# Performance work log

Measured on AMD Instinct MI355X. Metric: run time of the kernel, lower is better.

Reference implementation:

```python
import jax, jax.numpy as jnp
import numpy as np

D_MODEL = 768
D_STATE = 16
D_CONV = 4
EXPAND = 2
D_IN = D_MODEL // 2          # per-direction model dim = 384
D_INNER = EXPAND * D_IN      # ssm inner dim = 768
DT_RANK = (D_IN + 15) // 16  # 24 (mamba 'auto')
B, L = 2, 2048
EPS = 1e-5


def silu(x):
    return x * jax.nn.sigmoid(x)


def layernorm(x, w, b):
    m = jnp.mean(x, axis=-1, keepdims=True)
    v = jnp.var(x, axis=-1, keepdims=True)
    return (x - m) * jax.lax.rsqrt(v + EPS) * w + b


def causal_conv1d(u, w, b):
    # u: (B,L,di), w: (di,K) depthwise causal conv, b: (di,)
    K = w.shape[1]
    up = jnp.pad(u, ((0, 0), (K - 1, 0), (0, 0)))
    Lq = u.shape[1]
    y = sum(up[:, k:k + Lq, :] * w[:, k] for k in range(K))
    return y + b


def mamba_ssm(u, in_w, in_b, conv_w, conv_b, xp_w, dt_w, dt_b, A_log, Dp, out_w, out_b):
    # u: (B,L,D_IN)
    Bz = u.shape[0]
    xz = u @ in_w + in_b                         # (B,L,2*D_INNER)
    x, z = jnp.split(xz, 2, axis=-1)             # (B,L,D_INNER) each
    x = silu(causal_conv1d(x, conv_w, conv_b))
    xd = x @ xp_w                                # (B,L,DT_RANK+2N)
    dt = jax.nn.softplus(xd[..., :DT_RANK] @ dt_w + dt_b)   # (B,L,D_INNER)
    Bm = xd[..., DT_RANK:DT_RANK + D_STATE]      # (B,L,N)
    Cm = xd[..., DT_RANK + D_STATE:]             # (B,L,N)
    A = -jnp.exp(A_log)                          # (D_INNER,N)

    def step(h, xs):
        dt_t, x_t, B_t, C_t = xs                 # (B,di),(B,di),(B,N),(B,N)
        h = jnp.exp(dt_t[..., None] * A) * h + (dt_t * x_t)[..., None] * B_t[:, None, :]
        y = jnp.einsum('bdn,bn->bd', h, C_t)
        return h, y

    h0 = jnp.zeros((Bz, D_INNER, D_STATE), x.dtype)
    xs = (dt.transpose(1, 0, 2), x.transpose(1, 0, 2),
          Bm.transpose(1, 0, 2), Cm.transpose(1, 0, 2))
    _, ys = jax.lax.scan(step, h0, xs)           # ys: (L,B,D_INNER)
    y = ys.transpose(1, 0, 2) + x * Dp
    y = y * silu(z)
    return y @ out_w + out_b                     # (B,L,D_IN)


def setup_inputs() -> dict:
    key = jax.random.key(0)

    def nrm(i, shape, s=0.02):
        return jax.random.normal(jax.random.fold_in(key, i), shape, jnp.float32) * s

    d = {"x": jax.random.normal(jax.random.fold_in(key, 0), (B, L, D_MODEL), jnp.float32)}
    d["in_norm_w"] = jnp.ones(D_MODEL); d["in_norm_b"] = jnp.zeros(D_MODEL)
    d["ip_w"] = nrm(1, (D_MODEL, 2 * D_IN)); d["ip_b"] = jnp.zeros(2 * D_IN)
    i = 10
    for p in ("f", "b"):
        d[p + "_in_w"] = nrm(i, (D_IN, 2 * D_INNER)); d[p + "_in_b"] = jnp.zeros(2 * D_INNER)
        d[p + "_conv_w"] = nrm(i + 1, (D_INNER, D_CONV), 0.2); d[p + "_conv_b"] = jnp.zeros(D_INNER)
        d[p + "_xp_w"] = nrm(i + 2, (D_INNER, DT_RANK + 2 * D_STATE))
        d[p + "_dt_w"] = nrm(i + 3, (DT_RANK, D_INNER), 0.1)
        d[p + "_dt_b"] = nrm(i + 4, (D_INNER,), 0.5)
        d[p + "_A_log"] = jnp.log(jnp.tile(jnp.arange(1, D_STATE + 1, dtype=jnp.float32), (D_INNER, 1)))
        d[p + "_D"] = jnp.ones(D_INNER)
        d[p + "_out_w"] = nrm(i + 5, (D_INNER, D_IN)); d[p + "_out_b"] = jnp.zeros(D_IN)
        i += 10
    d["op_w"] = nrm(30, (2 * D_IN, D_MODEL)); d["op_b"] = jnp.zeros(D_MODEL)
    d["norm_w"] = jnp.ones(D_MODEL); d["norm_b"] = jnp.zeros(D_MODEL)
    return d


def reference(x, in_norm_w, in_norm_b, ip_w, ip_b,
              f_in_w, f_in_b, f_conv_w, f_conv_b, f_xp_w, f_dt_w, f_dt_b, f_A_log, f_D, f_out_w, f_out_b,
              b_in_w, b_in_b, b_conv_w, b_conv_b, b_xp_w, b_dt_w, b_dt_b, b_A_log, b_D, b_out_w, b_out_b,
              op_w, op_b, norm_w, norm_b):
    residual = x
    xn = layernorm(x, in_norm_w, in_norm_b)
    xp = xn @ ip_w + ip_b                        # (B,L,2*D_IN)
    x_fwd, x_bwd = jnp.split(xp, 2, axis=-1)
    out_fwd = mamba_ssm(x_fwd, f_in_w, f_in_b, f_conv_w, f_conv_b, f_xp_w,
                        f_dt_w, f_dt_b, f_A_log, f_D, f_out_w, f_out_b)
    out_bwd = mamba_ssm(jnp.flip(x_bwd, axis=1), b_in_w, b_in_b, b_conv_w, b_conv_b, b_xp_w,
                        b_dt_w, b_dt_b, b_A_log, b_D, b_out_w, b_out_b)
    out_bwd = jnp.flip(out_bwd, axis=1)
    out = jnp.concatenate([out_fwd, out_bwd], axis=-1) @ op_w + op_b
    # dropout is identity in eval mode
    return layernorm(residual + out, norm_w, norm_b)
```

## Files before the change

### kernel.cpp

```cpp
#include <hip/hip_runtime.h>
#include <hip/hip_bf16.h>
#include <math.h>
#include <type_traits>

#define BATCH 2
#define SEQ   2048
#define DMODEL 768
#define DIN   384
#define DINNER 768
#define DSTATE 16
#define DTRANK 24
#define ROWS  (BATCH*SEQ)
#define NCH   64
#define CLEN  (SEQ/NCH)

using short8  = __attribute__((ext_vector_type(8))) short;
using floatx4 = __attribute__((ext_vector_type(4))) float;

__device__ __forceinline__ ushort f2bf(float f) {
    union { float f; uint u; } v; v.f = f;
    uint r = (v.u + 0x7fffu + ((v.u >> 16) & 1u)) >> 16;
    return (ushort)r;
}
__device__ __forceinline__ float bf2f(ushort h) {
    union { uint u; float f; } v; v.u = ((uint)h) << 16;
    return v.f;
}
__device__ __forceinline__ void async16(const ushort* g, ushort* l) {
    __builtin_amdgcn_global_load_lds(
        (const __attribute__((address_space(1))) void*)g,
        (__attribute__((address_space(3))) void*)l,
        16, 0, 0);
}

template<int TM, int TN> struct GemmShT { ushort lA[TM * 64]; ushort lB[TN * 64]; };

template<int TM, int TN>
__device__ __forceinline__ void gemm_accum(
    const ushort* __restrict__ A, int lda,
    const ushort* __restrict__ Bt, int ldb,
    int K, int m0, int n0, GemmShT<TM, TN>& sh,
    floatx4 (&acc)[TM / 32][TN / 32])
{
    constexpr int WM = TM / 2, WN = TN / 2;
    constexpr int MT = WM / 16, NT = WN / 16;
    constexpr int AI = TM / 32, BI = TN / 32;
    const int tid = threadIdx.x;
    const int wave = tid >> 6, lane = tid & 63;
    const int wm = wave >> 1, wn = wave & 1;
    const int quad = lane >> 4, l16 = lane & 15;
    const int lrow = lane >> 3, lcol = (lane & 7) * 8;

    for (int k0 = 0; k0 < K; k0 += 64) {
#pragma unroll
        for (int i = 0; i < AI; i++) {
            int rb = (wave * AI + i) * 8;
            async16(A + (size_t)(m0 + rb + lrow) * lda + k0 + lcol, &sh.lA[rb * 64]);
        }
#pragma unroll
        for (int i = 0; i < BI; i++) {
            int rb = (wave * BI + i) * 8;
            async16(Bt + (size_t)(n0 + rb + lrow) * ldb + k0 + lcol, &sh.lB[rb * 64]);
        }
        __syncthreads();
#pragma unroll
        for (int ks = 0; ks < 2; ks++) {
            short8 af[MT], bf[NT];
#pragma unroll
            for (int i = 0; i < MT; i++)
                af[i] = *(const short8*)&sh.lA[(wm * WM + i * 16 + l16) * 64 + ks * 32 + quad * 8];
#pragma unroll
            for (int j = 0; j < NT; j++)
                bf[j] = *(const short8*)&sh.lB[(wn * WN + j * 16 + l16) * 64 + ks * 32 + quad * 8];
#pragma unroll
            for (int i = 0; i < MT; i++)
#pragma unroll
                for (int j = 0; j < NT; j++)
                    acc[i][j] = __builtin_amdgcn_mfma_f32_16x16x32_bf16(af[i], bf[j], acc[i][j], 0, 0, 0);
        }
        __syncthreads();
    }
}

template<int TM, int TN, bool OUT_BF>
__device__ __forceinline__ void gemm_epilogue(
    const float* __restrict__ bias, void* __restrict__ C, int ldc, int N,
    int m0, int n0, floatx4 (&acc)[TM / 32][TN / 32])
{
    constexpr int WM = TM / 2, WN = TN / 2;
    constexpr int MT = WM / 16, NT = WN / 16;
    const int tid = threadIdx.x;
    const int wave = tid >> 6, lane = tid & 63;
    const int wm = wave >> 1, wn = wave & 1;
    const int quad = lane >> 4, l16 = lane & 15;
#pragma unroll
    for (int i = 0; i < MT; i++) {
#pragma unroll
        for (int j = 0; j < NT; j++) {
            int row = m0 + wm * WM + i * 16 + quad * 4;
            int col = n0 + wn * WN + j * 16 + l16;
            if (col < N) {
                float bv = bias ? bias[col] : 0.f;
#pragma unroll
                for (int r = 0; r < 4; r++) {
                    float v = acc[i][j][r] + bv;
                    if (OUT_BF) ((ushort*)C)[(size_t)(row + r) * ldc + col] = f2bf(v);
                    else        ((float*)C)[(size_t)(row + r) * ldc + col] = v;
                }
            }
        }
    }
}

template<int TM, int TN, bool OUT_BF>
__global__ __launch_bounds__(256) void mfma_gemm_k(
    const ushort* __restrict__ A0, const ushort* __restrict__ A1, int lda,
    const ushort* __restrict__ B0, const ushort* __restrict__ B1, int ldb,
    const float* __restrict__ bias0, const float* __restrict__ bias1,
    void* __restrict__ C0, void* __restrict__ C1, int ldc, int N, int K)
{
    __shared__ GemmShT<TM, TN> sh;
    const ushort* A  = blockIdx.z ? A1 : A0;
    const ushort* Bt = blockIdx.z ? B1 : B0;
    const float* bias = blockIdx.z ? bias1 : bias0;
    void* C = blockIdx.z ? C1 : C0;
    floatx4 acc[TM / 32][TN / 32];
#pragma unroll
    for (int i = 0; i < TM / 32; i++)
#pragma unroll
        for (int j = 0; j < TN / 32; j++)
            acc[i][j] = (floatx4){0.f, 0.f, 0.f, 0.f};
    int m0 = blockIdx.y * TM, n0 = blockIdx.x * TN;
    gemm_accum<TM, TN>(A, lda, Bt, ldb, K, m0, n0, sh, acc);
    gemm_epilogue<TM, TN, OUT_BF>(bias, C, ldc, N, m0, n0, acc);
}

template<int TM, int TN>
__global__ __launch_bounds__(256) void outop_kernel(
    const ushort* __restrict__ A0, const ushort* __restrict__ B0,
    const ushort* __restrict__ A1, const ushort* __restrict__ B1,
    const float* __restrict__ bias, float* __restrict__ C,
    int lda, int ldb, int ldc, int N, int K)
{
    __shared__ GemmShT<TM, TN> sh;
    floatx4 acc[TM / 32][TN / 32];
#pragma unroll
    for (int i = 0; i < TM / 32; i++)
#pragma unroll
        for (int j = 0; j < TN / 32; j++)
            acc[i][j] = (floatx4){0.f, 0.f, 0.f, 0.f};
    int m0 = blockIdx.y * TM, n0 = blockIdx.x * TN;
    gemm_accum<TM, TN>(A0, lda, B0, ldb, K, m0, n0, sh, acc);
    gemm_accum<TM, TN>(A1, lda, B1, ldb, K, m0, n0, sh, acc);
    gemm_epilogue<TM, TN, false>(bias, (void*)C, ldc, N, m0, n0, acc);
}

struct LnSh { float ss[4]; float ssq[4]; float m; float rs; };

template<bool OUT_BF>
__device__ __forceinline__ void ln_row(
    int row, const float* __restrict__ x, const float* __restrict__ res,
    const float* __restrict__ w, const float* __restrict__ b,
    void* __restrict__ out, LnSh& sh)
{
    int tid = threadIdx.x;
    const float* xr = x + (size_t)row * DMODEL;
    const float* rr = res ? res + (size_t)row * DMODEL : nullptr;
    float v[3];
    float s = 0.f, sq = 0.f;
#pragma unroll
    for (int j = 0; j < 3; j++) {
        int i = tid + j * 256;
        float val = xr[i];
        if (rr) val += rr[i];
        v[j] = val; s += val; sq += val * val;
    }
#pragma unroll
    for (int off = 32; off; off >>= 1) {
        s  += __shfl_down(s,  off);
        sq += __shfl_down(sq, off);
    }
    int wid = tid >> 6;
    if ((tid & 63) == 0) { sh.ss[wid] = s; sh.ssq[wid] = sq; }
    __syncthreads();
    if (tid == 0) {
        float S  = sh.ss[0] + sh.ss[1] + sh.ss[2] + sh.ss[3];
        float SQ = sh.ssq[0] + sh.ssq[1] + sh.ssq[2] + sh.ssq[3];
        float m  = S * (1.0f / DMODEL);
        float var = SQ * (1.0f / DMODEL) - m * m;
        sh.m = m;
        sh.rs = rsqrtf(var + 1e-5f);
    }
    __syncthreads();
    float m = sh.m, rs = sh.rs;
#pragma unroll
    for (int j = 0; j < 3; j++) {
        int i = tid + j * 256;
        float r = (v[j] - m) * rs * w[i] + b[i];
        if (OUT_BF) ((ushort*)out)[(size_t)row * DMODEL + i] = f2bf(r);
        else        ((float*)out)[(size_t)row * DMODEL + i] = r;
    }
}

__global__ __launch_bounds__(256) void ln2_kernel(
    const float* __restrict__ x, const float* __restrict__ res,
    const float* __restrict__ w, const float* __restrict__ b,
    float* __restrict__ out)
{
    __shared__ LnSh sh;
    ln_row<false>(blockIdx.x, x, res, w, b, (void*)out, sh);
}

struct TD { const float* src; ushort* dst; int K, N, Np, tile0, tk, mode; };
struct PrepArgs {
    TD d[8];
    int ntc;
    const float *x, *in_nw, *in_nb;
    ushort* xn;
};

__global__ __launch_bounds__(256) void prep_kernel(PrepArgs p)
{
    __shared__ union { float tile[32][33]; LnSh l; } sh;
    int bi = blockIdx.x;
    if (bi < p.ntc) {
        int i = 0;
        while (i < 7 && bi >= p.d[i + 1].tile0) i++;
        TD t = p.d[i];
        int local = bi - t.tile0;
        int tki = local % t.tk, tn = local / t.tk;
        int k0 = tki * 32, n0 = tn * 32;
        if (t.mode == 0) {
            int tx = threadIdx.x & 31, ty = threadIdx.x >> 5;
#pragma unroll
            for (int r = ty; r < 32; r += 8) {
                int n = n0 + tx;
                sh.tile[r][tx] = (n < t.N) ? t.src[(size_t)(k0 + r) * t.N + n] : 0.f;
            }
            __syncthreads();
#pragma unroll
            for (int r = ty; r < 32; r += 8) {
                int n = n0 + r, k = k0 + tx;
                t.dst[(size_t)n * t.K + k] = f2bf(sh.tile[tx][r]);
            }
        } else {
#pragma unroll
            for (int e = threadIdx.x; e < 1024; e += 256) {
                int r = e >> 5, c = e & 31;
                size_t o = (size_t)(k0 + r) * t.N + n0 + c;
                t.dst[o] = f2bf(t.src[o]);
            }
        }
    } else {
        ln_row<true>(bi - p.ntc, p.x, (const float*)nullptr, p.in_nw, p.in_nb,
                     (void*)p.xn, sh.l);
    }
}

struct WfArgs {
    const ushort *fin, *bin, *opT, *ipc, *fow, *bow;
    ushort *WzF, *WzB, *WoF, *WoB;
    const float *ip_b, *f_in_b, *b_in_b, *f_out_b, *b_out_b, *op_b;
    const float *f_in_w32, *b_in_w32, *op_w32;
    float *bzf, *bzb, *bo;
};

__global__ __launch_bounds__(256) void wfuse_kernel(WfArgs p)
{
    __shared__ GemmShT<128, 64> sh;
    int t = blockIdx.x;
    if (t < 432) {
        const ushort *A, *Bt; ushort* C; int lda, ldb, m0, n0;
        if (t < 144)      { A = p.fin;       lda = 384; Bt = p.ipc;       ldb = 768; C = p.WzF; int u = t;       m0 = (u / 12) * 128; n0 = (u % 12) * 64; }
        else if (t < 288) { A = p.bin;       lda = 384; Bt = p.ipc + 384; ldb = 768; C = p.WzB; int u = t - 144; m0 = (u / 12) * 128; n0 = (u % 12) * 64; }
        else if (t < 360) { A = p.opT;       lda = 768; Bt = p.fow;       ldb = 384; C = p.WoF; int u = t - 288; m0 = (u / 12) * 128; n0 = (u % 12) * 64; }
        else              { A = p.opT + 384; lda = 768; Bt = p.bow;       ldb = 384; C = p.WoB; int u = t - 360; m0 = (u / 12) * 128; n0 = (u % 12) * 64; }
        floatx4 acc[4][2];
#pragma unroll
        for (int i = 0; i < 4; i++)
#pragma unroll
            for (int j = 0; j < 2; j++)
                acc[i][j] = (floatx4){0.f, 0.f, 0.f, 0.f};
        gemm_accum<128, 64>(A, lda, Bt, ldb, 384, m0, n0, sh, acc);
        gemm_epilogue<128, 64, true>((const float*)nullptr, (void*)C, 768, 768, m0, n0, acc);
    } else if (t < 438) {
        int n = (t - 432) * 256 + threadIdx.x;
        float acc = p.f_in_b[n];
        for (int j = 0; j < 384; j++)
            acc = fmaf(p.ip_b[j], p.f_in_w32[(size_t)j * 1536 + n], acc);
        p.bzf[n] = acc;
    } else if (t < 444) {
        int n = (t - 438) * 256 + threadIdx.x;
        float acc = p.b_in_b[n];
        for (int j = 0; j < 384; j++)
            acc = fmaf(p.ip_b[384 + j], p.b_in_w32[(size_t)j * 1536 + n], acc);
        p.bzb[n] = acc;
    } else {
        int n = (t - 444) * 256 + threadIdx.x;
        float acc = p.op_b[n];
        for (int j = 0; j < 384; j++)
            acc = fmaf(p.f_out_b[j], p.op_w32[(size_t)j * 768 + n], acc);
        for (int j = 0; j < 384; j++)
            acc = fmaf(p.b_out_b[j], p.op_w32[(size_t)(384 + j) * 768 + n], acc);
        p.bo[n] = acc;
    }
}

__global__ __launch_bounds__(256) void conv_silu_kernel(
    const ushort* __restrict__ xzf, const ushort* __restrict__ xzb,
    const float* __restrict__ cwf, const float* __restrict__ cbf,
    const float* __restrict__ cwb, const float* __restrict__ cbb,
    ushort* __restrict__ outf, ushort* __restrict__ outb)
{
    int rev = blockIdx.y;
    const ushort* xz = rev ? xzb : xzf;
    const float* cw = rev ? cwb : cwf;
    const float* cb = rev ? cbb : cbf;
    ushort* out = rev ? outb : outf;

    int idx = blockIdx.x * 256 + threadIdx.x;
    int dg = idx % (DINNER / 8);
    int row = idx / (DINNER / 8);
    int d0 = dg * 8;
    int t = row & (SEQ - 1), b = row >> 11;
    float acc[8];
#pragma unroll
    for (int c = 0; c < 8; c++) acc[c] = cb[d0 + c];
#pragma unroll
    for (int k = 0; k < 4; k++) {
        int ts = rev ? (t + 3 - k) : (t - 3 + k);
        if (ts >= 0 && ts < SEQ) {
            short8 v = *(const short8*)&xz[((size_t)(b * SEQ + ts)) * 1536 + d0];
#pragma unroll
            for (int c = 0; c < 8; c++)
                acc[c] = fmaf(cw[(d0 + c) * 4 + k], bf2f((ushort)v[c]), acc[c]);
        }
    }
    short8 o;
#pragma unroll
    for (int c = 0; c < 8; c++) {
        float sig = 1.f / (1.f + __expf(-acc[c]));
        o[c] = (short)f2bf(acc[c] * sig);
    }
    *(short8*)&out[(size_t)row * DINNER + d0] = o;
}

#define BM 64
#define BN 64
#define BK 16
__global__ __launch_bounds__(256) void dt_gemm_kernel(
    const float* __restrict__ A0f, const float* __restrict__ A1f, int lda,
    const float* __restrict__ W0, const float* __restrict__ W1, int ldw,
    const float* __restrict__ bias0, const float* __restrict__ bias1,
    float* __restrict__ C0f, float* __restrict__ C1f, int ldc, int K)
{
    const float* A = blockIdx.z ? A1f : A0f;
    const float* W = blockIdx.z ? W1 : W0;
    const float* bias = blockIdx.z ? bias1 : bias0;
    float* C = blockIdx.z ? C1f : C0f;

    __shared__ float As[BK][BM + 4];
    __shared__ float Bs[BK][BN + 4];
    int tid = threadIdx.x;
    int m0 = blockIdx.y * BM;
    int n0 = blockIdx.x * BN;
    int tx = tid & 15, ty = tid >> 4;
    float acc[4][4] = {};

    for (int k0 = 0; k0 < K; k0 += BK) {
        {
            int row = tid >> 2;
            int kq  = (tid & 3) * 4;
            const float* ap = A + (size_t)(m0 + row) * lda + k0 + kq;
            As[kq + 0][row] = (k0 + kq + 0 < K) ? ap[0] : 0.f;
            As[kq + 1][row] = (k0 + kq + 1 < K) ? ap[1] : 0.f;
            As[kq + 2][row] = (k0 + kq + 2 < K) ? ap[2] : 0.f;
            As[kq + 3][row] = (k0 + kq + 3 < K) ? ap[3] : 0.f;
        }
        {
            int krow = tid >> 4;
            int col  = (tid & 15) * 4;
            float4 wv = make_float4(0.f, 0.f, 0.f, 0.f);
            if (k0 + krow < K)
                wv = *(const float4*)(W + (size_t)(k0 + krow) * ldw + n0 + col);
            *(float4*)&Bs[krow][col] = wv;
        }
        __syncthreads();
#pragma unroll
        for (int k = 0; k < BK; k++) {
            float a[4], bv[4];
            *(float4*)a  = *(const float4*)&As[k][ty * 4];
            *(float4*)bv = *(const float4*)&Bs[k][tx * 4];
#pragma unroll
            for (int i = 0; i < 4; i++)
#pragma unroll
                for (int j = 0; j < 4; j++)
                    acc[i][j] = fmaf(a[i], bv[j], acc[i][j]);
        }
        __syncthreads();
    }
#pragma unroll
    for (int i = 0; i < 4; i++) {
        int m = m0 + ty * 4 + i;
#pragma unroll
        for (int j = 0; j < 4; j++) {
            int n = n0 + tx * 4 + j;
            float v = acc[i][j] + bias[n];
            v = (v > 20.f) ? v : log1pf(__expf(v));
            C[(size_t)m * ldc + n] = v;
        }
    }
}

template<bool FULL>
__global__ __launch_bounds__(256) void scan_chunk_kernel(
    const float* __restrict__ dtf, const ushort* __restrict__ xcf,
    const float* __restrict__ xdf, const ushort* __restrict__ xzf,
    const float* __restrict__ Alf, const float* __restrict__ Dff,
    const float* __restrict__ dtb, const ushort* __restrict__ xcb,
    const float* __restrict__ xdb, const ushort* __restrict__ xzb,
    const float* __restrict__ Alb, const float* __restrict__ Dbb,
    float* __restrict__ Hloc, float* __restrict__ Wp,
    const float* __restrict__ Hin,
    ushort* __restrict__ yf, ushort* __restrict__ yb)
{
    const int d     = blockIdx.x * 256 + threadIdx.x;
    const int chunk = blockIdx.y;
    const int bz    = blockIdx.z;
    const int dir   = bz >> 1;
    const int bat   = bz & 1;

    const float*  dt = dir ? dtb : dtf;
    const ushort* xc = dir ? xcb : xcf;
    const float*  xd = dir ? xdb : xdf;
    const ushort* xz = dir ? xzb : xzf;
    const float*  Al = dir ? Alb : Alf;
    const float*  Dp = dir ? Dbb : Dff;
    ushort* yo = dir ? yb : yf;

    float a[16];
    {
        const float4* Ap = (const float4*)(Al + (size_t)d * 16);
#pragma unroll
        for (int q = 0; q < 4; q++) {
            float4 v = Ap[q];
            a[q*4+0] = -__expf(v.x); a[q*4+1] = -__expf(v.y);
            a[q*4+2] = -__expf(v.z); a[q*4+3] = -__expf(v.w);
        }
    }
    const float a0 = a[0];
    bool fast = true;
#pragma unroll
    for (int n = 0; n < 16; n++) {
        float ideal = a0 * (float)(n + 1);
        fast = fast && (fabsf(a[n] - ideal) <= 1e-4f * fabsf(ideal) + 1e-7f);
    }

    float h[16];
    if (FULL) {
        size_t base = ((size_t)(bz * NCH + chunk) * DINNER + d) * 16;
#pragma unroll
        for (int q = 0; q < 4; q++) {
            float4 v = *(const float4*)(Hin + base + q * 4);
            h[q*4+0] = v.x; h[q*4+1] = v.y; h[q*4+2] = v.z; h[q*4+3] = v.w;
        }
    } else {
#pragma unroll
        for (int n = 0; n < 16; n++) h[n] = 0.f;
    }

    const float Dd = FULL ? Dp[d] : 0.f;
    float S = 0.f;

    auto run = [&](auto FASTC) {
        constexpr bool FAST = decltype(FASTC)::value;
#pragma unroll 2
        for (int i = 0; i < CLEN; i++) {
            int tl = chunk * CLEN + i;
            int t  = dir ? (SEQ - 1 - tl) : tl;
            size_t r = (size_t)(bat * SEQ + t);
            float dtv = dt[r * DINNER + d];
            float xv  = bf2f(xc[r * DINNER + d]);
            const float* bp = xd + r * 56 + DTRANK;
            float4 B0 = *(const float4*)(bp + 0);
            float4 B1 = *(const float4*)(bp + 4);
            float4 B2 = *(const float4*)(bp + 8);
            float4 B3 = *(const float4*)(bp + 12);
            float Bv[16] = {B0.x,B0.y,B0.z,B0.w, B1.x,B1.y,B1.z,B1.w,
                            B2.x,B2.y,B2.z,B2.w, B3.x,B3.y,B3.z,B3.w};
            float w[16];
            if (FAST) {
                float e1 = __expf(dtv * a0);
                float e2 = e1*e1, e4 = e2*e2, e8 = e4*e4;
                w[0]=e1;      w[1]=e2;      w[2]=e2*e1;   w[3]=e4;
                w[4]=e4*e1;   w[5]=e4*e2;   w[6]=e4*w[2]; w[7]=e8;
                w[8]=e8*e1;   w[9]=e8*e2;   w[10]=e8*w[2];w[11]=e8*e4;
                w[12]=e8*w[4];w[13]=e8*w[5];w[14]=e8*w[6];w[15]=e8*e8;
            } else {
#pragma unroll
                for (int n = 0; n < 16; n++) w[n] = __expf(dtv * a[n]);
            }
            float bx = dtv * xv;
#pragma unroll
            for (int n = 0; n < 16; n++)
                h[n] = fmaf(w[n], h[n], bx * Bv[n]);
            S += dtv;
            if (FULL) {
                const float* cp = bp + DSTATE;
                float4 C0 = *(const float4*)(cp + 0);
                float4 C1 = *(const float4*)(cp + 4);
                float4 C2 = *(const float4*)(cp + 8);
                float4 C3 = *(const float4*)(cp + 12);
                float Cv[16] = {C0.x,C0.y,C0.z,C0.w, C1.x,C1.y,C1.z,C1.w,
                                C2.x,C2.y,C2.z,C2.w, C3.x,C3.y,C3.z,C3.w};
                float y = 0.f;
#pragma unroll
                for (int n = 0; n < 16; n++) y = fmaf(h[n], Cv[n], y);
                float zv = bf2f(xz[r * 1536 + DINNER + d]);
                float sig = 1.f / (1.f + __expf(-zv));
                yo[r * DINNER + d] = f2bf((y + xv * Dd) * (zv * sig));
            }
        }
    };
    if (fast) run(std::true_type{}); else run(std::false_type{});

    if (!FULL) {
        float W[16];
        if (fast) {
            float E1 = __expf(S * a0);
            float E2 = E1*E1, E4 = E2*E2, E8 = E4*E4;
            W[0]=E1;      W[1]=E2;      W[2]=E2*E1;   W[3]=E4;
            W[4]=E4*E1;   W[5]=E4*E2;   W[6]=E4*W[2]; W[7]=E8;
            W[8]=E8*E1;   W[9]=E8*E2;   W[10]=E8*W[2];W[11]=E8*E4;
            W[12]=E8*W[4];W[13]=E8*W[5];W[14]=E8*W[6];W[15]=E8*E8;
        } else {
#pragma unroll
            for (int n = 0; n < 16; n++) W[n] = __expf(S * a[n]);
        }
        size_t base = ((size_t)(bz * NCH + chunk) * DINNER + d) * 16;
#pragma unroll
        for (int q = 0; q < 4; q++) {
            *(float4*)(Hloc + base + q*4) = make_float4(h[q*4+0], h[q*4+1], h[q*4+2], h[q*4+3]);
            *(float4*)(Wp   + base + q*4) = make_float4(W[q*4+0], W[q*4+1], W[q*4+2], W[q*4+3]);
        }
    }
}

__global__ __launch_bounds__(256) void scan_combine(
    const float* __restrict__ Hloc, const float* __restrict__ Wp,
    float* __restrict__ Hin)
{
    int idx = blockIdx.x * 256 + threadIdx.x;
    int bz = idx / (DINNER * 16);
    int rest = idx % (DINNER * 16);
    float hin = 0.f;
#pragma unroll 4
    for (int k = 0; k < NCH; k++) {
        size_t o = (size_t)(bz * NCH + k) * (DINNER * 16) + rest;
        Hin[o] = hin;
        hin = fmaf(Wp[o], hin, Hloc[o]);
    }
}

extern "C" void kernel_launch(void* const* d_in, const int* in_sizes, int n_in,
                              void* d_out, int out_size, void* d_ws, size_t ws_size,
                              hipStream_t stream)
{
    const float* x        = (const float*)d_in[0];
    const float* in_nw    = (const float*)d_in[1];
    const float* in_nb    = (const float*)d_in[2];
    const float* ip_w     = (const float*)d_in[3];
    const float* ip_b     = (const float*)d_in[4];
    const float* f_in_w   = (const float*)d_in[5];
    const float* f_in_b   = (const float*)d_in[6];
    const float* f_conv_w = (const float*)d_in[7];
    const float* f_conv_b = (const float*)d_in[8];
    const float* f_xp_w   = (const float*)d_in[9];
    const float* f_dt_w   = (const float*)d_in[10];
    const float* f_dt_b   = (const float*)d_in[11];
    const float* f_A_log  = (const float*)d_in[12];
    const float* f_D      = (const float*)d_in[13];
    const float* f_out_w  = (const float*)d_in[14];
    const float* f_out_b  = (const float*)d_in[15];
    const float* b_in_w   = (const float*)d_in[16];
    const float* b_in_b   = (const float*)d_in[17];
    const float* b_conv_w = (const float*)d_in[18];
    const float* b_conv_b = (const float*)d_in[19];
    const float* b_xp_w   = (const float*)d_in[20];
    const float* b_dt_w   = (const float*)d_in[21];
    const float* b_dt_b   = (const float*)d_in[22];
    const float* b_A_log  = (const float*)d_in[23];
    const float* b_D      = (const float*)d_in[24];
    const float* b_out_w  = (const float*)d_in[25];
    const float* b_out_b  = (const float*)d_in[26];
    const float* op_w     = (const float*)d_in[27];
    const float* op_b     = (const float*)d_in[28];
    const float* norm_w   = (const float*)d_in[29];
    const float* norm_b   = (const float*)d_in[30];

    size_t off = 0;
    auto alloc = [&](size_t bytes) {
        void* p = (char*)d_ws + off;
        off += (bytes + 255) & ~(size_t)255;
        return p;
    };
    const size_t R = ROWS;
    ushort* xn_bf   = (ushort*)alloc(R * 768 * 2);
    ushort* xz_f_bf = (ushort*)alloc(R * 1536 * 2);
    ushort* xz_b_bf = (ushort*)alloc(R * 1536 * 2);
    ushort* xc_f_bf = (ushort*)alloc(R * 768 * 2);
    ushort* xc_b_bf = (ushort*)alloc(R * 768 * 2);
    float*  xd_f    = (float*)alloc(R * 56 * 4);
    float*  xd_b    = (float*)alloc(R * 56 * 4);
    float*  dt_f    = (float*)alloc(R * 768 * 4);
    float*  dt_b    = (float*)alloc(R * 768 * 4);
    ushort* y_f_bf  = (ushort*)alloc(R * 768 * 2);
    ushort* y_b_bf  = (ushort*)alloc(R * 768 * 2);
    float*  outraw  = (float*)alloc(R * 768 * 4);
    const size_t SCN = (size_t)4 * NCH * DINNER * 16;
    float* Hloc = (float*)alloc(SCN * 4);
    float* Wpb  = (float*)alloc(SCN * 4);
    float* Hin  = (float*)alloc(SCN * 4);
    ushort* Wt_fin = (ushort*)alloc((size_t)1536 * 384 * 2);
    ushort* Wt_bin = (ushort*)alloc((size_t)1536 * 384 * 2);
    ushort* Wt_op  = (ushort*)alloc((size_t)768 * 768 * 2);
    ushort* Wt_fxp = (ushort*)alloc((size_t)64 * 768 * 2);
    ushort* Wt_bxp = (ushort*)alloc((size_t)64 * 768 * 2);
    ushort* ipc    = (ushort*)alloc((size_t)768 * 768 * 2);
    ushort* fow    = (ushort*)alloc((size_t)768 * 384 * 2);
    ushort* bow    = (ushort*)alloc((size_t)768 * 384 * 2);
    ushort* WzF    = (ushort*)alloc((size_t)1536 * 768 * 2);
    ushort* WzB    = (ushort*)alloc((size_t)1536 * 768 * 2);
    ushort* WoF    = (ushort*)alloc((size_t)768 * 768 * 2);
    ushort* WoB    = (ushort*)alloc((size_t)768 * 768 * 2);
    float*  bzf    = (float*)alloc(1536 * 4);
    float*  bzb    = (float*)alloc(1536 * 4);
    float*  bo     = (float*)alloc(768 * 4);

    PrepArgs pa;
    int tile0 = 0, nd = 0;
    auto add = [&](const float* s, ushort* dst, int K, int N, int Np, int mode) {
        int tiles = mode == 0 ? (K / 32) * (Np / 32) : (K / 32) * (N / 32);
        pa.d[nd] = TD{s, dst, K, N, Np, tile0, K / 32, mode};
        tile0 += tiles;
        nd++;
    };
    add(f_in_w,  Wt_fin, 384, 1536, 1536, 0);
    add(b_in_w,  Wt_bin, 384, 1536, 1536, 0);
    add(op_w,    Wt_op,  768, 768, 768, 0);
    add(f_xp_w,  Wt_fxp, 768, 56, 64, 0);
    add(b_xp_w,  Wt_bxp, 768, 56, 64, 0);
    add(ip_w,    ipc,    768, 768, 768, 1);
    add(f_out_w, fow,    768, 384, 384, 1);
    add(b_out_w, bow,    768, 384, 384, 1);
    pa.ntc = tile0;
    pa.x = x; pa.in_nw = in_nw; pa.in_nb = in_nb; pa.xn = xn_bf;
    hipLaunchKernelGGL(prep_kernel, dim3(tile0 + ROWS), dim3(256), 0, stream, pa);

    WfArgs wa;
    wa.fin = Wt_fin; wa.bin = Wt_bin; wa.opT = Wt_op;
    wa.ipc = ipc; wa.fow = fow; wa.bow = bow;
    wa.WzF = WzF; wa.WzB = WzB; wa.WoF = WoF; wa.WoB = WoB;
    wa.ip_b = ip_b; wa.f_in_b = f_in_b; wa.b_in_b = b_in_b;
    wa.f_out_b = f_out_b; wa.b_out_b = b_out_b; wa.op_b = op_b;
    wa.f_in_w32 = f_in_w; wa.b_in_w32 = b_in_w; wa.op_w32 = op_w;
    wa.bzf = bzf; wa.bzb = bzb; wa.bo = bo;
    hipLaunchKernelGGL(wfuse_kernel, dim3(447), dim3(256), 0, stream, wa);

    hipLaunchKernelGGL((mfma_gemm_k<128, 128, true>), dim3(12, 32, 2), dim3(256), 0, stream,
                       xn_bf, xn_bf, 768, WzF, WzB, 768, bzf, bzb,
                       (void*)xz_f_bf, (void*)xz_b_bf, 1536, 1536, 768);

    hipLaunchKernelGGL(conv_silu_kernel, dim3(ROWS * DINNER / 8 / 256, 2), dim3(256), 0, stream,
                       xz_f_bf, xz_b_bf, f_conv_w, f_conv_b, b_conv_w, b_conv_b,
                       xc_f_bf, xc_b_bf);

    hipLaunchKernelGGL((mfma_gemm_k<128, 64, false>), dim3(1, 32, 2), dim3(256), 0, stream,
                       xc_f_bf, xc_b_bf, 768, Wt_fxp, Wt_bxp, 768,
                       (const float*)nullptr, (const float*)nullptr,
                       (void*)xd_f, (void*)xd_b, 56, 56, 768);

    hipLaunchKernelGGL(dt_gemm_kernel, dim3(768 / BN, ROWS / BM, 2), dim3(256), 0, stream,
                       xd_f, xd_b, 56, f_dt_w, b_dt_w, 768, f_dt_b, b_dt_b,
                       dt_f, dt_b, 768, DTRANK);

    hipLaunchKernelGGL((scan_chunk_kernel<false>), dim3(DINNER / 256, NCH, 4), dim3(256), 0, stream,
                       dt_f, xc_f_bf, xd_f, xz_f_bf, f_A_log, f_D,
                       dt_b, xc_b_bf, xd_b, xz_b_bf, b_A_log, b_D,
                       Hloc, Wpb, (const float*)nullptr, (ushort*)nullptr, (ushort*)nullptr);
    hipLaunchKernelGGL(scan_combine, dim3(4 * DINNER * 16 / 256), dim3(256), 0, stream,
                       Hloc, Wpb, Hin);
    hipLaunchKernelGGL((scan_chunk_kernel<true>), dim3(DINNER / 256, NCH, 4), dim3(256), 0, stream,
                       dt_f, xc_f_bf, xd_f, xz_f_bf, f_A_log, f_D,
                       dt_b, xc_b_bf, xd_b, xz_b_bf, b_A_log, b_D,
                       (float*)nullptr, (float*)nullptr, Hin, y_f_bf, y_b_bf);

    hipLaunchKernelGGL((outop_kernel<128, 64>), dim3(12, 32), dim3(256), 0, stream,
                       y_f_bf, WoF, y_b_bf, WoB, bo, outraw, 768, 768, 768, 768, 768);

    hipLaunchKernelGGL(ln2_kernel, dim3(ROWS), dim3(256), 0, stream,
                       x, outraw, norm_w, norm_b, (float*)d_out);
}
```

Baseline: 401.7 us.

## Fold dt projection into x_proj GEMM, swizzle LDS, and rescalarize conv

Precomputes a combined weight (xp_w columns plus xp_w·dt_w) so a single MFMA GEMM produces both xd and the dt pre-activation, with softplus applied in its epilogue. This removes the separate fp32 SIMT dt GEMM launch and its re-read of xd. The GEMM tile loader and LDS reads gain an XOR swizzle meant to avoid shared-memory bank conflicts. The conv+SiLU kernel changes from eight channels per thread with vector loads to one channel per thread, which lowers per-thread work but adds more and narrower memory accesses. Computing dt through bf16 combined weights changes numerical precision.

```diff
diff --git a/kernel.cpp b/kernel.cpp
--- a/kernel.cpp
+++ b/kernel.cpp
@@ -49,7 +49,8 @@
     const int wave = tid >> 6, lane = tid & 63;
     const int wm = wave >> 1, wn = wave & 1;
     const int quad = lane >> 4, l16 = lane & 15;
-    const int lrow = lane >> 3, lcol = (lane & 7) * 8;
+    const int lrow = lane >> 3;
+    const int lcol = ((lane & 7) ^ (lane >> 3)) * 8;
 
     for (int k0 = 0; k0 < K; k0 += 64) {
 #pragma unroll
@@ -67,11 +68,15 @@
         for (int ks = 0; ks < 2; ks++) {
             short8 af[MT], bf[NT];
 #pragma unroll
-            for (int i = 0; i < MT; i++)
-                af[i] = *(const short8*)&sh.lA[(wm * WM + i * 16 + l16) * 64 + ks * 32 + quad * 8];
-#pragma unroll
-            for (int j = 0; j < NT; j++)
-                bf[j] = *(const short8*)&sh.lB[(wn * WN + j * 16 + l16) * 64 + ks * 32 + quad * 8];
+            for (int i = 0; i < MT; i++) {
+                int row = wm * WM + i * 16 + l16;
+                af[i] = *(const short8*)&sh.lA[row * 64 + ((ks * 4 + quad) ^ (row & 7)) * 8];
+            }
+#pragma unroll
+            for (int j = 0; j < NT; j++) {
+                int row = wn * WN + j * 16 + l16;
+                bf[j] = *(const short8*)&sh.lB[row * 64 + ((ks * 4 + quad) ^ (row & 7)) * 8];
+            }
 #pragma unroll
             for (int i = 0; i < MT; i++)
 #pragma unroll
@@ -133,6 +138,56 @@
     int m0 = blockIdx.y * TM, n0 = blockIdx.x * TN;
     gemm_accum<TM, TN>(A, lda, Bt, ldb, K, m0, n0, sh, acc);
     gemm_epilogue<TM, TN, OUT_BF>(bias, C, ldc, N, m0, n0, acc);
+}
+
+__global__ __launch_bounds__(256) void xddt_kernel(
+    const ushort* __restrict__ xcf, const ushort* __restrict__ xcb,
+    const ushort* __restrict__ Wcf, const ushort* __restrict__ Wcb,
+    const float* __restrict__ dtbf, const float* __restrict__ dtbb,
+    float* __restrict__ xdf, float* __restrict__ xdb,
+    float* __restrict__ dtf, float* __restrict__ dtb)
+{
+    constexpr int TM = 128, TN = 64;
+    __shared__ GemmShT<TM, TN> sh;
+    const ushort* A  = blockIdx.z ? xcb : xcf;
+    const ushort* Bt = blockIdx.z ? Wcb : Wcf;
+    const float* dbias = blockIdx.z ? dtbb : dtbf;
+    float* xd = blockIdx.z ? xdb : xdf;
+    float* dt = blockIdx.z ? dtb : dtf;
+    floatx4 acc[4][2];
+#pragma unroll
+    for (int i = 0; i < 4; i++)
+#pragma unroll
+        for (int j = 0; j < 2; j++)
+            acc[i][j] = (floatx4){0.f, 0.f, 0.f, 0.f};
+    int m0 = blockIdx.y * TM, n0 = blockIdx.x * TN;
+    gemm_accum<TM, TN>(A, 768, Bt, 768, 768, m0, n0, sh, acc);
+    const int tid = threadIdx.x;
+    const int wave = tid >> 6, lane = tid & 63;
+    const int wm = wave >> 1, wn = wave & 1;
+    const int quad = lane >> 4, l16 = lane & 15;
+#pragma unroll
+    for (int i = 0; i < 4; i++) {
+#pragma unroll
+        for (int j = 0; j < 2; j++) {
+            int row = m0 + wm * 64 + i * 16 + quad * 4;
+            int col = n0 + wn * 32 + j * 16 + l16;
+            if (col < 56) {
+#pragma unroll
+                for (int r = 0; r < 4; r++)
+                    xd[(size_t)(row + r) * 56 + col] = acc[i][j][r];
+            } else if (col >= 64) {
+                int jj = col - 64;
+                float bv = dbias[jj];
+#pragma unroll
+                for (int r = 0; r < 4; r++) {
+                    float v = acc[i][j][r] + bv;
+                    v = (v > 20.f) ? v : log1pf(__expf(v));
+                    dt[(size_t)(row + r) * 768 + jj] = v;
+                }
+            }
+        }
+    }
 }
 
 template<int TM, int TN>
@@ -211,9 +266,9 @@
     ln_row<false>(blockIdx.x, x, res, w, b, (void*)out, sh);
 }
 
-struct TD { const float* src; ushort* dst; int K, N, Np, tile0, tk, mode; };
+struct TD { const float* src; ushort* dst; int K, N, Kp, Np, ldd, tile0, tkp, mode; };
 struct PrepArgs {
-    TD d[8];
+    TD d[12];
     int ntc;
     const float *x, *in_nw, *in_nb;
     ushort* xn;
@@ -225,30 +280,31 @@
     int bi = blockIdx.x;
     if (bi < p.ntc) {
         int i = 0;
-        while (i < 7 && bi >= p.d[i + 1].tile0) i++;
+        while (i < 11 && bi >= p.d[i + 1].tile0) i++;
         TD t = p.d[i];
         int local = bi - t.tile0;
-        int tki = local % t.tk, tn = local / t.tk;
+        int tki = local % t.tkp, tn = local / t.tkp;
         int k0 = tki * 32, n0 = tn * 32;
         if (t.mode == 0) {
             int tx = threadIdx.x & 31, ty = threadIdx.x >> 5;
 #pragma unroll
             for (int r = ty; r < 32; r += 8) {
-                int n = n0 + tx;
-                sh.tile[r][tx] = (n < t.N) ? t.src[(size_t)(k0 + r) * t.N + n] : 0.f;
+                int k = k0 + r, n = n0 + tx;
+                sh.tile[r][tx] = (k < t.K && n < t.N) ? t.src[(size_t)k * t.N + n] : 0.f;
             }
             __syncthreads();
 #pragma unroll
             for (int r = ty; r < 32; r += 8) {
                 int n = n0 + r, k = k0 + tx;
-                t.dst[(size_t)n * t.K + k] = f2bf(sh.tile[tx][r]);
+                t.dst[(size_t)n * t.ldd + k] = f2bf(sh.tile[tx][r]);
             }
         } else {
 #pragma unroll
             for (int e = threadIdx.x; e < 1024; e += 256) {
                 int r = e >> 5, c = e & 31;
-                size_t o = (size_t)(k0 + r) * t.N + n0 + c;
-                t.dst[o] = f2bf(t.src[o]);
+                int k = k0 + r, n = n0 + c;
+                float v = (k < t.K && n < t.N) ? t.src[(size_t)k * t.N + n] : 0.f;
+                t.dst[(size_t)k * t.ldd + n] = f2bf(v);
             }
         }
     } else {
@@ -259,7 +315,8 @@
 
 struct WfArgs {
     const ushort *fin, *bin, *opT, *ipc, *fow, *bow;
-    ushort *WzF, *WzB, *WoF, *WoB;
+    const ushort *dtwTf, *dtwTb, *xpcf, *xpcb;
+    ushort *WzF, *WzB, *WoF, *WoB, *WcF, *WcB;
     const float *ip_b, *f_in_b, *b_in_b, *f_out_b, *b_out_b, *op_b;
     const float *f_in_w32, *b_in_w32, *op_w32;
     float *bzf, *bzb, *bo;
@@ -269,34 +326,36 @@
 {
     __shared__ GemmShT<128, 64> sh;
     int t = blockIdx.x;
-    if (t < 432) {
-        const ushort *A, *Bt; ushort* C; int lda, ldb, m0, n0;
-        if (t < 144)      { A = p.fin;       lda = 384; Bt = p.ipc;       ldb = 768; C = p.WzF; int u = t;       m0 = (u / 12) * 128; n0 = (u % 12) * 64; }
-        else if (t < 288) { A = p.bin;       lda = 384; Bt = p.ipc + 384; ldb = 768; C = p.WzB; int u = t - 144; m0 = (u / 12) * 128; n0 = (u % 12) * 64; }
-        else if (t < 360) { A = p.opT;       lda = 768; Bt = p.fow;       ldb = 384; C = p.WoF; int u = t - 288; m0 = (u / 12) * 128; n0 = (u % 12) * 64; }
-        else              { A = p.opT + 384; lda = 768; Bt = p.bow;       ldb = 384; C = p.WoB; int u = t - 360; m0 = (u / 12) * 128; n0 = (u % 12) * 64; }
+    if (t < 576) {
+        const ushort *A, *Bt; ushort* C; int lda, ldb, K, m0, n0;
+        if (t < 144)      { A = p.fin;   lda = 384; Bt = p.ipc;       ldb = 768; K = 384; C = p.WzF;           int u = t;       m0 = (u / 12) * 128; n0 = (u % 12) * 64; }
+        else if (t < 288) { A = p.bin;   lda = 384; Bt = p.ipc + 384; ldb = 768; K = 384; C = p.WzB;           int u = t - 144; m0 = (u / 12) * 128; n0 = (u % 12) * 64; }
+        else if (t < 360) { A = p.opT;   lda = 768; Bt = p.fow;       ldb = 384; K = 384; C = p.WoF;           int u = t - 288; m0 = (u / 12) * 128; n0 = (u % 12) * 64; }
+        else if (t < 432) { A = p.opT + 384; lda = 768; Bt = p.bow;   ldb = 384; K = 384; C = p.WoB;           int u = t - 360; m0 = (u / 12) * 128; n0 = (u % 12) * 64; }
+        else if (t < 504) { A = p.dtwTf; lda = 64;  Bt = p.xpcf;      ldb = 64;  K = 64;  C = p.WcF + 64*768;  int u = t - 432; m0 = (u / 12) * 128; n0 = (u % 12) * 64; }
+        else              { A = p.dtwTb; lda = 64;  Bt = p.xpcb;      ldb = 64;  K = 64;  C = p.WcB + 64*768;  int u = t - 504; m0 = (u / 12) * 128; n0 = (u % 12) * 64; }
         floatx4 acc[4][2];
 #pragma unroll
         for (int i = 0; i < 4; i++)
 #pragma unroll
             for (int j = 0; j < 2; j++)
                 acc[i][j] = (floatx4){0.f, 0.f, 0.f, 0.f};
-        gemm_accum<128, 64>(A, lda, Bt, ldb, 384, m0, n0, sh, acc);
+        gemm_accum<128, 64>(A, lda, Bt, ldb, K, m0, n0, sh, acc);
         gemm_epilogue<128, 64, true>((const float*)nullptr, (void*)C, 768, 768, m0, n0, acc);
-    } else if (t < 438) {
-        int n = (t - 432) * 256 + threadIdx.x;
+    } else if (t < 582) {
+        int n = (t - 576) * 256 + threadIdx.x;
         float acc = p.f_in_b[n];
         for (int j = 0; j < 384; j++)
             acc = fmaf(p.ip_b[j], p.f_in_w32[(size_t)j * 1536 + n], acc);
         p.bzf[n] = acc;
-    } else if (t < 444) {
-        int n = (t - 438) * 256 + threadIdx.x;
+    } else if (t < 588) {
+        int n = (t - 582) * 256 + threadIdx.x;
         float acc = p.b_in_b[n];
         for (int j = 0; j < 384; j++)
             acc = fmaf(p.ip_b[384 + j], p.b_in_w32[(size_t)j * 1536 + n], acc);
         p.bzb[n] = acc;
     } else {
-        int n = (t - 444) * 256 + threadIdx.x;
+        int n = (t - 588) * 256 + threadIdx.x;
         float acc = p.op_b[n];
         for (int j = 0; j < 384; j++)
             acc = fmaf(p.f_out_b[j], p.op_w32[(size_t)j * 768 + n], acc);
@@ -319,97 +378,20 @@
     ushort* out = rev ? outb : outf;
 
     int idx = blockIdx.x * 256 + threadIdx.x;
-    int dg = idx % (DINNER / 8);
-    int row = idx / (DINNER / 8);
-    int d0 = dg * 8;
+    int d = idx % DINNER;
+    int row = idx / DINNER;
     int t = row & (SEQ - 1), b = row >> 11;
-    float acc[8];
-#pragma unroll
-    for (int c = 0; c < 8; c++) acc[c] = cb[d0 + c];
+    float4 w4 = *(const float4*)&cw[d * 4];
+    float wk[4] = {w4.x, w4.y, w4.z, w4.w};
+    float acc = cb[d];
 #pragma unroll
     for (int k = 0; k < 4; k++) {
         int ts = rev ? (t + 3 - k) : (t - 3 + k);
-        if (ts >= 0 && ts < SEQ) {
-            short8 v = *(const short8*)&xz[((size_t)(b * SEQ + ts)) * 1536 + d0];
-#pragma unroll
-            for (int c = 0; c < 8; c++)
-                acc[c] = fmaf(cw[(d0 + c) * 4 + k], bf2f((ushort)v[c]), acc[c]);
-        }
-    }
-    short8 o;
-#pragma unroll
-    for (int c = 0; c < 8; c++) {
-        float sig = 1.f / (1.f + __expf(-acc[c]));
-        o[c] = (short)f2bf(acc[c] * sig);
-    }
-    *(short8*)&out[(size_t)row * DINNER + d0] = o;
-}
-
-#define BM 64
-#define BN 64
-#define BK 16
-__global__ __launch_bounds__(256) void dt_gemm_kernel(
-    const float* __restrict__ A0f, const float* __restrict__ A1f, int lda,
-    const float* __restrict__ W0, const float* __restrict__ W1, int ldw,
-    const float* __restrict__ bias0, const float* __restrict__ bias1,
-    float* __restrict__ C0f, float* __restrict__ C1f, int ldc, int K)
-{
-    const float* A = blockIdx.z ? A1f : A0f;
-    const float* W = blockIdx.z ? W1 : W0;
-    const float* bias = blockIdx.z ? bias1 : bias0;
-    float* C = blockIdx.z ? C1f : C0f;
-
-    __shared__ float As[BK][BM + 4];
-    __shared__ float Bs[BK][BN + 4];
-    int tid = threadIdx.x;
-    int m0 = blockIdx.y * BM;
-    int n0 = blockIdx.x * BN;
-    int tx = tid & 15, ty = tid >> 4;
-    float acc[4][4] = {};
-
-    for (int k0 = 0; k0 < K; k0 += BK) {
-        {
-            int row = tid >> 2;
-            int kq  = (tid & 3) * 4;
-            const float* ap = A + (size_t)(m0 + row) * lda + k0 + kq;
-            As[kq + 0][row] = (k0 + kq + 0 < K) ? ap[0] : 0.f;
-            As[kq + 1][row] = (k0 + kq + 1 < K) ? ap[1] : 0.f;
-            As[kq + 2][row] = (k0 + kq + 2 < K) ? ap[2] : 0.f;
-            As[kq + 3][row] = (k0 + kq + 3 < K) ? ap[3] : 0.f;
-        }
-        {
-            int krow = tid >> 4;
-            int col  = (tid & 15) * 4;
-            float4 wv = make_float4(0.f, 0.f, 0.f, 0.f);
-            if (k0 + krow < K)
-                wv = *(const float4*)(W + (size_t)(k0 + krow) * ldw + n0 + col);
-            *(float4*)&Bs[krow][col] = wv;
-        }
-        __syncthreads();
-#pragma unroll
-        for (int k = 0; k < BK; k++) {
-            float a[4], bv[4];
-            *(float4*)a  = *(const float4*)&As[k][ty * 4];
-            *(float4*)bv = *(const float4*)&Bs[k][tx * 4];
-#pragma unroll
-            for (int i = 0; i < 4; i++)
-#pragma unroll
-                for (int j = 0; j < 4; j++)
-                    acc[i][j] = fmaf(a[i], bv[j], acc[i][j]);
-        }
-        __syncthreads();
-    }
-#pragma unroll
-    for (int i = 0; i < 4; i++) {
-        int m = m0 + ty * 4 + i;
-#pragma unroll
-        for (int j = 0; j < 4; j++) {
-            int n = n0 + tx * 4 + j;
-            float v = acc[i][j] + bias[n];
-            v = (v > 20.f) ? v : log1pf(__expf(v));
-            C[(size_t)m * ldc + n] = v;
-        }
-    }
+        if (ts >= 0 && ts < SEQ)
+            acc = fmaf(wk[k], bf2f(xz[((size_t)(b * SEQ + ts)) * 1536 + d]), acc);
+    }
+    float sig = 1.f / (1.f + __expf(-acc));
+    out[idx] = f2bf(acc * sig);
 }
 
 template<bool FULL>
@@ -624,35 +606,43 @@
     ushort* Wt_fin = (ushort*)alloc((size_t)1536 * 384 * 2);
     ushort* Wt_bin = (ushort*)alloc((size_t)1536 * 384 * 2);
     ushort* Wt_op  = (ushort*)alloc((size_t)768 * 768 * 2);
-    ushort* Wt_fxp = (ushort*)alloc((size_t)64 * 768 * 2);
-    ushort* Wt_bxp = (ushort*)alloc((size_t)64 * 768 * 2);
     ushort* ipc    = (ushort*)alloc((size_t)768 * 768 * 2);
     ushort* fow    = (ushort*)alloc((size_t)768 * 384 * 2);
     ushort* bow    = (ushort*)alloc((size_t)768 * 384 * 2);
+    ushort* dtwT_f = (ushort*)alloc((size_t)768 * 64 * 2);
+    ushort* dtwT_b = (ushort*)alloc((size_t)768 * 64 * 2);
+    ushort* xpc_f  = (ushort*)alloc((size_t)768 * 64 * 2);
+    ushort* xpc_b  = (ushort*)alloc((size_t)768 * 64 * 2);
     ushort* WzF    = (ushort*)alloc((size_t)1536 * 768 * 2);
     ushort* WzB    = (ushort*)alloc((size_t)1536 * 768 * 2);
     ushort* WoF    = (ushort*)alloc((size_t)768 * 768 * 2);
     ushort* WoB    = (ushort*)alloc((size_t)768 * 768 * 2);
+    ushort* WcF    = (ushort*)alloc((size_t)832 * 768 * 2);
+    ushort* WcB    = (ushort*)alloc((size_t)832 * 768 * 2);
     float*  bzf    = (float*)alloc(1536 * 4);
     float*  bzb    = (float*)alloc(1536 * 4);
     float*  bo     = (float*)alloc(768 * 4);
 
     PrepArgs pa;
     int tile0 = 0, nd = 0;
-    auto add = [&](const float* s, ushort* dst, int K, int N, int Np, int mode) {
-        int tiles = mode == 0 ? (K / 32) * (Np / 32) : (K / 32) * (N / 32);
-        pa.d[nd] = TD{s, dst, K, N, Np, tile0, K / 32, mode};
-        tile0 += tiles;
+    auto add = [&](const float* s, ushort* dst, int K, int N, int Kp, int Np,
+                   int ldd, int mode) {
+        pa.d[nd] = TD{s, dst, K, N, Kp, Np, ldd, tile0, Kp / 32, mode};
+        tile0 += (Kp / 32) * (Np / 32);
         nd++;
     };
-    add(f_in_w,  Wt_fin, 384, 1536, 1536, 0);
-    add(b_in_w,  Wt_bin, 384, 1536, 1536, 0);
-    add(op_w,    Wt_op,  768, 768, 768, 0);
-    add(f_xp_w,  Wt_fxp, 768, 56, 64, 0);
-    add(b_xp_w,  Wt_bxp, 768, 56, 64, 0);
-    add(ip_w,    ipc,    768, 768, 768, 1);
-    add(f_out_w, fow,    768, 384, 384, 1);
-    add(b_out_w, bow,    768, 384, 384, 1);
+    add(f_in_w,  Wt_fin,      384, 1536, 384, 1536, 384, 0);
+    add(b_in_w,  Wt_bin,      384, 1536, 384, 1536, 384, 0);
+    add(op_w,    Wt_op,       768, 768,  768, 768,  768, 0);
+    add(f_xp_w,  WcF,         768, 56,   768, 64,   768, 0);
+    add(b_xp_w,  WcB,         768, 56,   768, 64,   768, 0);
+    add(f_dt_w,  dtwT_f,      24,  768,  64,  768,  64,  0);
+    add(b_dt_w,  dtwT_b,      24,  768,  64,  768,  64,  0);
+    add(ip_w,    ipc,         768, 768,  768, 768,  768, 1);
+    add(f_out_w, fow,         768, 384,  768, 384,  384, 1);
+    add(b_out_w, bow,         768, 384,  768, 384,  384, 1);
+    add(f_xp_w,  xpc_f,       768, 56,   768, 64,   64,  1);
+    add(b_xp_w,  xpc_b,       768, 56,   768, 64,   64,  1);
     pa.ntc = tile0;
     pa.x = x; pa.in_nw = in_nw; pa.in_nb = in_nb; pa.xn = xn_bf;
     hipLaunchKernelGGL(prep_kernel, dim3(tile0 + ROWS), dim3(256), 0, stream, pa);
@@ -660,29 +650,25 @@
     WfArgs wa;
     wa.fin = Wt_fin; wa.bin = Wt_bin; wa.opT = Wt_op;
     wa.ipc = ipc; wa.fow = fow; wa.bow = bow;
-    wa.WzF = WzF; wa.WzB = WzB; wa.WoF = WoF; wa.WoB = WoB;
+    wa.dtwTf = dtwT_f; wa.dtwTb = dtwT_b; wa.xpcf = xpc_f; wa.xpcb = xpc_b;
+    wa.WzF = WzF; wa.WzB = WzB; wa.WoF = WoF; wa.WoB = WoB; wa.WcF = WcF; wa.WcB = WcB;
     wa.ip_b = ip_b; wa.f_in_b = f_in_b; wa.b_in_b = b_in_b;
     wa.f_out_b = f_out_b; wa.b_out_b = b_out_b; wa.op_b = op_b;
     wa.f_in_w32 = f_in_w; wa.b_in_w32 = b_in_w; wa.op_w32 = op_w;
     wa.bzf = bzf; wa.bzb = bzb; wa.bo = bo;
-    hipLaunchKernelGGL(wfuse_kernel, dim3(447), dim3(256), 0, stream, wa);
+    hipLaunchKernelGGL(wfuse_kernel, dim3(591), dim3(256), 0, stream, wa);
 
     hipLaunchKernelGGL((mfma_gemm_k<128, 128, true>), dim3(12, 32, 2), dim3(256), 0, stream,
                        xn_bf, xn_bf, 768, WzF, WzB, 768, bzf, bzb,
                        (void*)xz_f_bf, (void*)xz_b_bf, 1536, 1536, 768);
 
-    hipLaunchKernelGGL(conv_silu_kernel, dim3(ROWS * DINNER / 8 / 256, 2), dim3(256), 0, stream,
+    hipLaunchKernelGGL(conv_silu_kernel, dim3(ROWS * DINNER / 256, 2), dim3(256), 0, stream,
                        xz_f_bf, xz_b_bf, f_conv_w, f_conv_b, b_conv_w, b_conv_b,
                        xc_f_bf, xc_b_bf);
 
-    hipLaunchKernelGGL((mfma_gemm_k<128, 64, false>), dim3(1, 32, 2), dim3(256), 0, stream,
-                       xc_f_bf, xc_b_bf, 768, Wt_fxp, Wt_bxp, 768,
-                       (const float*)nullptr, (const float*)nullptr,
-                       (void*)xd_f, (void*)xd_b, 56, 56, 768);
-
-    hipLaunchKernelGGL(dt_gemm_kernel, dim3(768 / BN, ROWS / BM, 2), dim3(256), 0, stream,
-                       xd_f, xd_b, 56, f_dt_w, b_dt_w, 768, f_dt_b, b_dt_b,
-                       dt_f, dt_b, 768, DTRANK);
+    hipLaunchKernelGGL(xddt_kernel, dim3(13, 32, 2), dim3(256), 0, stream,
+                       xc_f_bf, xc_b_bf, WcF, WcB, f_dt_b, b_dt_b,
+                       xd_f, xd_b, dt_f, dt_b);
 
     hipLaunchKernelGGL((scan_chunk_kernel<false>), dim3(DINNER / 256, NCH, 4), dim3(256), 0, stream,
                        dt_f, xc_f_bf, xd_f, xz_f_bf, f_A_log, f_D,
```

Measured after the change: 364.9 us. 1.1x faster.
